# Kernel tuning notes

Measured on AMD Instinct MI355X. Metric: run time of the kernel, lower is better.

Reference implementation:

```python
import jax, jax.numpy as jnp
import numpy as np

NEG_INF = -1e30


def setup_inputs() -> dict:
    key = jax.random.key(0)
    ks = jax.random.split(key, 6)
    B, S, D, H, DK = 32, 512, 512, 8, 64
    x = jax.random.normal(ks[0], (B, S, D), dtype=jnp.float32)
    mask = jax.random.randint(ks[1], (B, S), 0, 2, dtype=jnp.int32)
    # xavier-uniform-like scale for [D, DK] projections
    lim_qkv = float(np.sqrt(6.0 / (D + DK)))
    lim_o = float(np.sqrt(6.0 / (D + D)))
    Wq = jax.random.uniform(ks[2], (H, D, DK), jnp.float32, -lim_qkv, lim_qkv)
    Wk = jax.random.uniform(ks[3], (H, D, DK), jnp.float32, -lim_qkv, lim_qkv)
    Wv = jax.random.uniform(ks[4], (H, D, DK), jnp.float32, -lim_qkv, lim_qkv)
    Wo = jax.random.uniform(ks[5], (D, D), jnp.float32, -lim_o, lim_o)
    bias = jnp.zeros((1,), dtype=jnp.float32)
    return {"x": x, "mask": mask, "Wq": Wq, "Wk": Wk, "Wv": Wv, "Wo": Wo, "bias": bias}


def reference(x, mask, Wq, Wk, Wv, Wo, bias):
    B, S, D = x.shape
    H, _, DK = Wq.shape
    scale = 1.0 / jnp.sqrt(jnp.float32(DK))
    # Fused per-head QKV projections (original loops over heads)
    Q = jnp.einsum("bsd,hdk->bhsk", x, Wq) + bias  # [B,H,S,DK]
    K = jnp.einsum("bsd,hdk->bhsk", x, Wk) + bias
    V = jnp.einsum("bsd,hdk->bhsk", x, Wv) + bias
    scores = jnp.einsum("bhsk,bhtk->bhst", Q, K) * scale  # [B,H,S,S]
    # CS224N masked_softmax: mask*logits + (1-mask)*(-1e30), softmax over keys
    m = mask.astype(scores.dtype)[:, None, None, :]  # [B,1,1,S]
    masked = m * scores + (1.0 - m) * NEG_INF
    probs = jax.nn.softmax(masked, axis=-1)
    heads = jnp.einsum("bhst,bhtv->bhsv", probs, V)  # [B,H,S,DK]
    multihead = heads.transpose(0, 2, 1, 3).reshape(B, S, H * DK)  # concat heads
    out = jnp.matmul(multihead, Wo) + bias  # [B,S,D]
    return out
```

## Files before the change

kernel.cpp:

```cpp
#include <hip/hip_runtime.h>
#include <hip/hip_bf16.h>
#include <math.h>

#define NB 32
#define NS 512
#define ND 512
#define NH 8
#define NDK 64

typedef __attribute__((ext_vector_type(8))) short bfrag;
typedef __attribute__((ext_vector_type(4))) float f32x4;

#define SCL 0.18033688011112042592f

__device__ __forceinline__ ushort f2bf(float f) {
    union { float f; unsigned u; } v; v.f = f;
    unsigned u = v.u;
    return (ushort)((u + 0x7fffu + ((u >> 16) & 1u)) >> 16);
}

__device__ __forceinline__ unsigned pk2bf(float a, float b) {
    __hip_bfloat162 h = __float22bfloat162_rn(make_float2(a, b));
    return *reinterpret_cast<unsigned*>(&h);
}

__device__ __forceinline__ void async16(const ushort* g, ushort* l) {
    __builtin_amdgcn_global_load_lds(
        (const __attribute__((address_space(1))) unsigned int*)g,
        (__attribute__((address_space(3))) unsigned int*)l, 16, 0, 0);
}

__global__ __launch_bounds__(256) void prep(const float* __restrict__ x,
                                            const float* __restrict__ Wq,
                                            const float* __restrict__ Wk,
                                            const float* __restrict__ Wv,
                                            const float* __restrict__ Wo,
                                            ushort* __restrict__ xb,
                                            ushort* __restrict__ WT,
                                            ushort* __restrict__ WoT) {
    __shared__ ushort T[64 * 72];
    const int tid = threadIdx.x;
    if (blockIdx.x < 8192) {
        const int idx = blockIdx.x * 256 + tid;
        const float4 v = reinterpret_cast<const float4*>(x)[idx];
        ushort4 o;
        o.x = f2bf(v.x); o.y = f2bf(v.y); o.z = f2bf(v.z); o.w = f2bf(v.w);
        reinterpret_cast<ushort4*>(xb)[idx] = o;
        return;
    }
    const int bid = blockIdx.x - 8192;
    const float* src; ushort* dst; int d0, n0, stride;
    if (bid < 192) {
        const int which = bid >> 6, h = (bid >> 3) & 7, rt = bid & 7;
        const float* Ws = (which == 0) ? Wq : (which == 1) ? Wk : Wv;
        src = Ws + (size_t)h * ND * NDK;
        dst = WT + (size_t)(which * NH + h) * NDK * ND;
        d0 = rt * 64; n0 = 0; stride = NDK;
    } else {
        const int t = bid - 192, rt = t >> 3, ct = t & 7;
        src = Wo; dst = WoT;
        d0 = rt * 64; n0 = ct * 64; stride = ND;
    }
    #pragma unroll
    for (int i = 0; i < 4; i++) {
        const int u = i * 256 + tid;
        const int row = u >> 4, cq = u & 15;
        const float4 v = *reinterpret_cast<const float4*>(&src[(size_t)(d0 + row) * stride + n0 + cq * 4]);
        T[(cq * 4 + 0) * 72 + row] = f2bf(v.x);
        T[(cq * 4 + 1) * 72 + row] = f2bf(v.y);
        T[(cq * 4 + 2) * 72 + row] = f2bf(v.z);
        T[(cq * 4 + 3) * 72 + row] = f2bf(v.w);
    }
    __syncthreads();
    #pragma unroll
    for (int i = 0; i < 2; i++) {
        const int u = i * 256 + tid;
        const int n = u >> 3, dq = u & 7;
        *reinterpret_cast<float4*>(&dst[(size_t)(n0 + n) * ND + d0 + dq * 8]) =
            *reinterpret_cast<float4*>(&T[n * 72 + dq * 8]);
    }
}

__global__ __launch_bounds__(256) void proj(const ushort* __restrict__ xb,
                                            const ushort* __restrict__ WT,
                                            const float* __restrict__ bias,
                                            ushort* __restrict__ QKb,
                                            ushort* __restrict__ VT) {
    __shared__ ushort sm[20480];
    const int tid = threadIdx.x;
    const int w = tid >> 6, lane = tid & 63, quad = lane >> 4, l16 = lane & 15;
    const int lr = lane >> 3, lc = lane & 7, cs = lc ^ lr, swz = l16 & 7;
    const float bb = bias[0];

    f32x4 acc[4][4];
    #pragma unroll
    for (int i = 0; i < 4; i++)
        #pragma unroll
        for (int j = 0; j < 4; j++) acc[i][j] = (f32x4){0.f, 0.f, 0.f, 0.f};

    if (blockIdx.x < 1024) {
        ushort* As = sm;
        ushort* Bs = sm + 8192;
        const int bid = blockIdx.x;
        const int m0 = (bid & 127) * 128, n0 = (bid >> 7) * 128;
        const int rw = (w & 1) * 64, cw = (w >> 1) * 64;
        for (int d0 = 0; d0 < ND; d0 += 64) {
            __syncthreads();
            #pragma unroll
            for (int t = 0; t < 4; t++) {
                const int rb = (w * 4 + t) * 8;
                async16(&xb[(size_t)(m0 + rb + lr) * ND + d0 + cs * 8], &As[rb * 64]);
                const int slot = rb + lr, nn = slot & 63;
                const int j = n0 + (slot & 64) + 4 * (nn & 15) + (nn >> 4);
                async16(&WT[(size_t)j * ND + d0 + cs * 8], &Bs[rb * 64]);
            }
            __syncthreads();
            #pragma unroll
            for (int ks = 0; ks < 2; ks++) {
                const int ch = ((ks * 4 + quad) ^ swz) * 8;
                bfrag a[4], bo[4];
                #pragma unroll
                for (int rf = 0; rf < 4; rf++) a[rf] = *(const bfrag*)&As[(rw + rf * 16 + l16) * 64 + ch];
                #pragma unroll
                for (int cf = 0; cf < 4; cf++) bo[cf] = *(const bfrag*)&Bs[(cw + cf * 16 + l16) * 64 + ch];
                #pragma unroll
                for (int rf = 0; rf < 4; rf++)
                    #pragma unroll
                    for (int cf = 0; cf < 4; cf++)
                        acc[rf][cf] = __builtin_amdgcn_mfma_f32_16x16x32_bf16(a[rf], bo[cf], acc[rf][cf], 0, 0, 0);
            }
        }
        #pragma unroll
        for (int rf = 0; rf < 4; rf++)
            #pragma unroll
            for (int r = 0; r < 4; r++) {
                const int row = m0 + rw + rf * 16 + quad * 4 + r;
                uint2 u;
                u.x = pk2bf(acc[rf][0][r] + bb, acc[rf][1][r] + bb);
                u.y = pk2bf(acc[rf][2][r] + bb, acc[rf][3][r] + bb);
                *(uint2*)&QKb[(size_t)row * 1024 + n0 + cw + 4 * l16] = u;
            }
    } else {
        ushort* As = sm;
        ushort* Bs = sm + 4096;
        const int bid = blockIdx.x - 1024;
        const int bh = bid >> 1, s0 = (bid & 1) * 256;
        const int b = bh >> 3, h = bh & 7;
        const int cw = w * 64;
        const ushort* Av = WT + (size_t)(2 * NH + h) * NDK * ND;
        const ushort* xrow = xb + (size_t)b * NS * ND;
        for (int d0 = 0; d0 < ND; d0 += 64) {
            __syncthreads();
            #pragma unroll
            for (int t = 0; t < 2; t++) {
                const int rb = w * 16 + t * 8;
                async16(&Av[(size_t)(rb + lr) * ND + d0 + cs * 8], &As[rb * 64]);
            }
            #pragma unroll
            for (int t = 0; t < 8; t++) {
                const int rb = (w * 8 + t) * 8;
                const int slot = rb + lr, nn = slot & 63;
                const int js = s0 + (slot & 192) + 4 * (nn & 15) + (nn >> 4);
                async16(&xrow[(size_t)js * ND + d0 + cs * 8], &Bs[rb * 64]);
            }
            __syncthreads();
            #pragma unroll
            for (int ks = 0; ks < 2; ks++) {
                const int ch = ((ks * 4 + quad) ^ swz) * 8;
                bfrag a[4], bo[4];
                #pragma unroll
                for (int rf = 0; rf < 4; rf++) a[rf] = *(const bfrag*)&As[(rf * 16 + l16) * 64 + ch];
                #pragma unroll
                for (int cf = 0; cf < 4; cf++) bo[cf] = *(const bfrag*)&Bs[(cw + cf * 16 + l16) * 64 + ch];
                #pragma unroll
                for (int rf = 0; rf < 4; rf++)
                    #pragma unroll
                    for (int cf = 0; cf < 4; cf++)
                        acc[rf][cf] = __builtin_amdgcn_mfma_f32_16x16x32_bf16(a[rf], bo[cf], acc[rf][cf], 0, 0, 0);
            }
        }
        ushort* vbase = VT + (size_t)bh * NDK * NS;
        #pragma unroll
        for (int rf = 0; rf < 4; rf++)
            #pragma unroll
            for (int r = 0; r < 4; r++) {
                const int dk = rf * 16 + quad * 4 + r;
                uint2 u;
                u.x = pk2bf(acc[rf][0][r] + bb, acc[rf][1][r] + bb);
                u.y = pk2bf(acc[rf][2][r] + bb, acc[rf][3][r] + bb);
                *(uint2*)&vbase[(size_t)dk * NS + s0 + cw + 4 * l16] = u;
            }
    }
}

__global__ __launch_bounds__(256) void attn_mfma(const ushort* __restrict__ QKb,
                                                 const ushort* __restrict__ VT,
                                                 const int* __restrict__ mask,
                                                 ushort* __restrict__ Hb) {
    __shared__ ushort QP[128 * 72];
    __shared__ ushort Ks[64 * 64];
    __shared__ ushort Vs[64 * 64];
    const int id = blockIdx.x;
    const int bh = id & 255, b = bh >> 3, h = bh & 7;
    const int s0 = (id >> 8) * 128;
    const int tid = threadIdx.x;
    const int w = tid >> 6, lane = tid & 63, quad = lane >> 4, l16 = lane & 15;
    const int lr = lane >> 3, lc = lane & 7, cs = lc ^ lr, swz = l16 & 7;

    const ushort* qbase = QKb + (size_t)(b * NS + s0) * 1024 + h * 64;
    const ushort* kbase = QKb + (size_t)(b * NS) * 1024 + 512 + h * 64;
    const ushort* vbase = VT + (size_t)(b * NH + h) * NDK * NS;

    #pragma unroll
    for (int t = 0; t < 4; t++) {
        const int rb = (w * 4 + t) * 8;
        async16(&qbase[(size_t)(rb + lr) * 1024 + cs * 8], &QP[rb * 64]);
    }
    __syncthreads();

    bfrag qf[2][2];
    #pragma unroll
    for (int ks = 0; ks < 2; ks++)
        #pragma unroll
        for (int rf = 0; rf < 2; rf++)
            qf[ks][rf] = *(const bfrag*)&QP[(w * 32 + rf * 16 + l16) * 64 + ((ks * 4 + quad) ^ swz) * 8];
    asm volatile("s_waitcnt lgkmcnt(0)" ::: "memory");
    __syncthreads();
    ushort* Ps = QP;

    bfrag ones;
    #pragma unroll
    for (int i = 0; i < 8; i++) ones[i] = (short)0x3F80;

    f32x4 acc_l[2];
    f32x4 acc_o[2][4];
    #pragma unroll
    for (int rf = 0; rf < 2; rf++) {
        acc_l[rf] = (f32x4){0.f, 0.f, 0.f, 0.f};
        #pragma unroll
        for (int c = 0; c < 4; c++) acc_o[rf][c] = (f32x4){0.f, 0.f, 0.f, 0.f};
    }

    for (int kt = 0; kt < 8; kt++) {
        __syncthreads();
        #pragma unroll
        for (int t = 0; t < 2; t++) {
            const int rb = (w * 2 + t) * 8;
            const int n = rb + lr;
            const int jk = 4 * (n & 15) + (n >> 4);
            async16(&kbase[(size_t)(kt * 64 + jk) * 1024 + cs * 8], &Ks[rb * 64]);
            async16(&vbase[(size_t)jk * NS + kt * 64 + cs * 8], &Vs[rb * 64]);
        }
        __syncthreads();

        f32x4 sc[2][4];
        #pragma unroll
        for (int rf = 0; rf < 2; rf++)
            #pragma unroll
            for (int c = 0; c < 4; c++) sc[rf][c] = (f32x4){0.f, 0.f, 0.f, 0.f};
        #pragma unroll
        for (int ks = 0; ks < 2; ks++) {
            const int ch = ((ks * 4 + quad) ^ swz) * 8;
            bfrag bo[4];
            #pragma unroll
            for (int c = 0; c < 4; c++) bo[c] = *(const bfrag*)&Ks[(c * 16 + l16) * 64 + ch];
            #pragma unroll
            for (int rf = 0; rf < 2; rf++)
                #pragma unroll
                for (int c = 0; c < 4; c++)
                    sc[rf][c] = __builtin_amdgcn_mfma_f32_16x16x32_bf16(qf[ks][rf], bo[c], sc[rf][c], 0, 0, 0);
        }

        const int4 mk4 = *(const int4*)&mask[b * NS + kt * 64 + 4 * l16];
        float mb[4];
        mb[0] = mk4.x ? 0.f : -INFINITY;
        mb[1] = mk4.y ? 0.f : -INFINITY;
        mb[2] = mk4.z ? 0.f : -INFINITY;
        mb[3] = mk4.w ? 0.f : -INFINITY;
        #pragma unroll
        for (int rf = 0; rf < 2; rf++) {
            #pragma unroll
            for (int c = 0; c < 4; c++)
                #pragma unroll
                for (int r = 0; r < 4; r++)
                    sc[rf][c][r] = exp2f(fmaf(sc[rf][c][r], SCL, mb[c]));
            #pragma unroll
            for (int r = 0; r < 4; r++) {
                uint2 u;
                u.x = pk2bf(sc[rf][0][r], sc[rf][1][r]);
                u.y = pk2bf(sc[rf][2][r], sc[rf][3][r]);
                *(uint2*)&Ps[(w * 32 + rf * 16 + quad * 4 + r) * 72 + l16 * 4] = u;
            }
        }

        #pragma unroll
        for (int ks = 0; ks < 2; ks++) {
            const int ch = ((ks * 4 + quad) ^ swz) * 8;
            bfrag bo[4];
            #pragma unroll
            for (int c = 0; c < 4; c++) bo[c] = *(const bfrag*)&Vs[(c * 16 + l16) * 64 + ch];
            #pragma unroll
            for (int rf = 0; rf < 2; rf++) {
                const bfrag a = *(const bfrag*)&Ps[(w * 32 + rf * 16 + l16) * 72 + ks * 32 + quad * 8];
                acc_l[rf] = __builtin_amdgcn_mfma_f32_16x16x32_bf16(a, ones, acc_l[rf], 0, 0, 0);
                #pragma unroll
                for (int c = 0; c < 4; c++)
                    acc_o[rf][c] = __builtin_amdgcn_mfma_f32_16x16x32_bf16(a, bo[c], acc_o[rf][c], 0, 0, 0);
            }
        }
    }

    ushort* hbase = Hb + (size_t)(b * NS + s0) * ND + h * 64;
    #pragma unroll
    for (int rf = 0; rf < 2; rf++)
        #pragma unroll
        for (int r = 0; r < 4; r++) {
            const float inv = 1.0f / acc_l[rf][r];
            const int row = w * 32 + rf * 16 + quad * 4 + r;
            uint2 u;
            u.x = pk2bf(acc_o[rf][0][r] * inv, acc_o[rf][1][r] * inv);
            u.y = pk2bf(acc_o[rf][2][r] * inv, acc_o[rf][3][r] * inv);
            *(uint2*)&hbase[(size_t)row * ND + 4 * l16] = u;
        }
}

__global__ __launch_bounds__(256) void out_gemm(const ushort* __restrict__ Hb,
                                                const ushort* __restrict__ WoT,
                                                const float* __restrict__ bias,
                                                float* __restrict__ out) {
    __shared__ ushort As[128 * 64];
    __shared__ ushort Bs[128 * 64];
    const int bid = blockIdx.x;
    const int m0 = (bid & 127) * 128, n0 = (bid >> 7) * 128;
    const int tid = threadIdx.x;
    const int w = tid >> 6, lane = tid & 63, quad = lane >> 4, l16 = lane & 15;
    const int lr = lane >> 3, lc = lane & 7, cs = lc ^ lr, swz = l16 & 7;
    const int rw = (w & 1) * 64, cw = (w >> 1) * 64;

    f32x4 acc[4][4];
    #pragma unroll
    for (int i = 0; i < 4; i++)
        #pragma unroll
        for (int j = 0; j < 4; j++) acc[i][j] = (f32x4){0.f, 0.f, 0.f, 0.f};

    for (int d0 = 0; d0 < ND; d0 += 64) {
        __syncthreads();
        #pragma unroll
        for (int t = 0; t < 4; t++) {
            const int rb = (w * 4 + t) * 8;
            async16(&Hb[(size_t)(m0 + rb + lr) * ND + d0 + cs * 8], &As[rb * 64]);
            const int slot = rb + lr, nn = slot & 63;
            const int j = n0 + (slot & 64) + 4 * (nn & 15) + (nn >> 4);
            async16(&WoT[(size_t)j * ND + d0 + cs * 8], &Bs[rb * 64]);
        }
        __syncthreads();
        #pragma unroll
        for (int ks = 0; ks < 2; ks++) {
            const int ch = ((ks * 4 + quad) ^ swz) * 8;
            bfrag a[4], bo[4];
            #pragma unroll
            for (int rf = 0; rf < 4; rf++) a[rf] = *(const bfrag*)&As[(rw + rf * 16 + l16) * 64 + ch];
            #pragma unroll
            for (int cf = 0; cf < 4; cf++) bo[cf] = *(const bfrag*)&Bs[(cw + cf * 16 + l16) * 64 + ch];
            #pragma unroll
            for (int rf = 0; rf < 4; rf++)
                #pragma unroll
                for (int cf = 0; cf < 4; cf++)
                    acc[rf][cf] = __builtin_amdgcn_mfma_f32_16x16x32_bf16(a[rf], bo[cf], acc[rf][cf], 0, 0, 0);
        }
    }

    const float bb = bias[0];
    #pragma unroll
    for (int rf = 0; rf < 4; rf++)
        #pragma unroll
        for (int r = 0; r < 4; r++) {
            const int row = m0 + rw + rf * 16 + quad * 4 + r;
            float4 v;
            v.x = acc[rf][0][r] + bb; v.y = acc[rf][1][r] + bb;
            v.z = acc[rf][2][r] + bb; v.w = acc[rf][3][r] + bb;
            *(float4*)&out[(size_t)row * ND + n0 + cw + 4 * l16] = v;
        }
}

extern "C" void kernel_launch(void* const* d_in, const int* in_sizes, int n_in,
                              void* d_out, int out_size, void* d_ws, size_t ws_size,
                              hipStream_t stream) {
    const float* x    = (const float*)d_in[0];
    const int*   mask = (const int*)  d_in[1];
    const float* Wq   = (const float*)d_in[2];
    const float* Wk   = (const float*)d_in[3];
    const float* Wv   = (const float*)d_in[4];
    const float* Wo   = (const float*)d_in[5];
    const float* bias = (const float*)d_in[6];
    float* out = (float*)d_out;

    const size_t TE = (size_t)NB * NS * ND;
    ushort* xb  = (ushort*)d_ws;
    ushort* WT  = xb  + TE;
    ushort* WoT = WT  + (size_t)3 * NH * NDK * ND;
    ushort* QKb = WoT + (size_t)ND * ND;
    ushort* VT  = QKb + (size_t)NB * NS * 2 * ND;
    ushort* Hb  = VT  + TE;

    prep<<<dim3(8448), dim3(256), 0, stream>>>(x, Wq, Wk, Wv, Wo, xb, WT, WoT);
    proj<<<dim3(1536), dim3(256), 0, stream>>>(xb, WT, bias, QKb, VT);
    attn_mfma<<<dim3(1024), dim3(256), 0, stream>>>(QKb, VT, mask, Hb);
    out_gemm<<<dim3(512), dim3(256), 0, stream>>>(Hb, WoT, bias, out);
}
```

Measured before the change: 190.1 us.

## Double-buffer K/V tiles in attention kernel to overlap loads with compute

Splits the K and V shared-memory tiles into two buffers. The first tile is prefetched together with Q, and each iteration issues async loads for the next tile before running the score and PV MFMAs on the current one. This replaces the two barriers per iteration with a single barrier at the end, so global-to-LDS latency is meant to hide behind compute. In exchange it doubles K/V LDS use, which may lower occupancy, and relies on the trailing barrier waiting for outstanding async loads.

```diff
diff --git a/kernel.cpp b/kernel.cpp
--- a/kernel.cpp
+++ b/kernel.cpp
@@ -198,8 +198,8 @@
                                                  const int* __restrict__ mask,
                                                  ushort* __restrict__ Hb) {
     __shared__ ushort QP[128 * 72];
-    __shared__ ushort Ks[64 * 64];
-    __shared__ ushort Vs[64 * 64];
+    __shared__ ushort Ks[2][64 * 64];
+    __shared__ ushort Vs[2][64 * 64];
     const int id = blockIdx.x;
     const int bh = id & 255, b = bh >> 3, h = bh & 7;
     const int s0 = (id >> 8) * 128;
@@ -211,11 +211,18 @@
     const ushort* kbase = QKb + (size_t)(b * NS) * 1024 + 512 + h * 64;
     const ushort* vbase = VT + (size_t)(b * NH + h) * NDK * NS;
 
+    const int rbA = (w * 2 + 0) * 8, nA = rbA + lr, jkA = 4 * (nA & 15) + (nA >> 4);
+    const int rbB = (w * 2 + 1) * 8, nB = rbB + lr, jkB = 4 * (nB & 15) + (nB >> 4);
+
     #pragma unroll
     for (int t = 0; t < 4; t++) {
         const int rb = (w * 4 + t) * 8;
         async16(&qbase[(size_t)(rb + lr) * 1024 + cs * 8], &QP[rb * 64]);
     }
+    async16(&kbase[(size_t)jkA * 1024 + cs * 8], &Ks[0][rbA * 64]);
+    async16(&kbase[(size_t)jkB * 1024 + cs * 8], &Ks[0][rbB * 64]);
+    async16(&vbase[(size_t)jkA * NS + cs * 8], &Vs[0][rbA * 64]);
+    async16(&vbase[(size_t)jkB * NS + cs * 8], &Vs[0][rbB * 64]);
     __syncthreads();
 
     bfrag qf[2][2];
@@ -241,17 +248,18 @@
         for (int c = 0; c < 4; c++) acc_o[rf][c] = (f32x4){0.f, 0.f, 0.f, 0.f};
     }
 
+    #pragma unroll 2
     for (int kt = 0; kt < 8; kt++) {
-        __syncthreads();
-        #pragma unroll
-        for (int t = 0; t < 2; t++) {
-            const int rb = (w * 2 + t) * 8;
-            const int n = rb + lr;
-            const int jk = 4 * (n & 15) + (n >> 4);
-            async16(&kbase[(size_t)(kt * 64 + jk) * 1024 + cs * 8], &Ks[rb * 64]);
-            async16(&vbase[(size_t)jk * NS + kt * 64 + cs * 8], &Vs[rb * 64]);
-        }
-        __syncthreads();
+        const int cur = kt & 1;
+        if (kt < 7) {
+            const int nxt = cur ^ 1;
+            const ushort* kb2 = kbase + (size_t)(kt + 1) * 64 * 1024;
+            const ushort* vb2 = vbase + (size_t)(kt + 1) * 64;
+            async16(&kb2[(size_t)jkA * 1024 + cs * 8], &Ks[nxt][rbA * 64]);
+            async16(&kb2[(size_t)jkB * 1024 + cs * 8], &Ks[nxt][rbB * 64]);
+            async16(&vb2[(size_t)jkA * NS + cs * 8], &Vs[nxt][rbA * 64]);
+            async16(&vb2[(size_t)jkB * NS + cs * 8], &Vs[nxt][rbB * 64]);
+        }
 
         f32x4 sc[2][4];
         #pragma unroll
@@ -263,7 +271,7 @@
             const int ch = ((ks * 4 + quad) ^ swz) * 8;
             bfrag bo[4];
             #pragma unroll
-            for (int c = 0; c < 4; c++) bo[c] = *(const bfrag*)&Ks[(c * 16 + l16) * 64 + ch];
+            for (int c = 0; c < 4; c++) bo[c] = *(const bfrag*)&Ks[cur][(c * 16 + l16) * 64 + ch];
             #pragma unroll
             for (int rf = 0; rf < 2; rf++)
                 #pragma unroll
@@ -298,7 +306,7 @@
             const int ch = ((ks * 4 + quad) ^ swz) * 8;
             bfrag bo[4];
             #pragma unroll
-            for (int c = 0; c < 4; c++) bo[c] = *(const bfrag*)&Vs[(c * 16 + l16) * 64 + ch];
+            for (int c = 0; c < 4; c++) bo[c] = *(const bfrag*)&Vs[cur][(c * 16 + l16) * 64 + ch];
             #pragma unroll
             for (int rf = 0; rf < 2; rf++) {
                 const bfrag a = *(const bfrag*)&Ps[(w * 32 + rf * 16 + l16) * 72 + ks * 32 + quad * 8];
@@ -308,6 +316,8 @@
                     acc_o[rf][c] = __builtin_amdgcn_mfma_f32_16x16x32_bf16(a, bo[c], acc_o[rf][c], 0, 0, 0);
             }
         }
+
+        if (kt < 7) __syncthreads();
     }
 
     ushort* hbase = Hb + (size_t)(b * NS + s0) * ND + h * 64;
```

Result: faster. 179.9 us (-5.3%).
